# Kernel tuning notes

Measured on AMD Instinct MI355X. Metric: run time of the kernel, lower is better.

## Reference

```python
import jax, jax.numpy as jnp
import numpy as np

B = 8192
I = 1024
H = 1024


def setup_inputs() -> dict:
    key = jax.random.key(0)
    ks = jax.random.split(key, 7)
    s_in = 1.0 / np.sqrt(I)
    s_h = 1.0 / np.sqrt(H)
    return {
        "x_current": jax.random.normal(ks[0], (B, I), dtype=jnp.float32),
        "c_previous": jax.random.normal(ks[1], (B, H), dtype=jnp.float32),
        "h_previous": jax.random.normal(ks[2], (B, H), dtype=jnp.float32),
        # stacked gate weights, order (i, f, o, g); equivalent to 8 small nn.Linear
        "Wx": jax.random.normal(ks[3], (4 * H, I), dtype=jnp.float32) * s_in,
        "bx": jax.random.normal(ks[4], (4 * H,), dtype=jnp.float32) * s_in,
        "Wh": jax.random.normal(ks[5], (4 * H, H), dtype=jnp.float32) * s_h,
        "bh": jax.random.normal(ks[6], (4 * H,), dtype=jnp.float32) * s_h,
    }


def reference(x_current, c_previous, h_previous, Wx, bx, Wh, bh):
    # two fused GEMMs covering all 8 original linears: [B, 4H]
    gates = (jnp.einsum("bi,gi->bg", x_current, Wx) + bx
             + jnp.einsum("bh,gh->bg", h_previous, Wh) + bh)
    i_g, f_g, o_g, g_g = jnp.split(gates, 4, axis=-1)
    input_gate = jax.nn.sigmoid(i_g)
    forget_gate = jax.nn.sigmoid(f_g)
    output_gate = jax.nn.sigmoid(o_g)
    g_current = jnp.tanh(g_g)
    c_current = forget_gate * c_previous + input_gate * g_current
    h_current = output_gate * jnp.tanh(c_current)
    return (c_current, h_current)
```

## Files before the change

### kernel.cpp

```cpp
#include <hip/hip_runtime.h>
#include <hip/hip_bf16.h>

#define Bsz 8192
#define Isz 1024
#define Hsz 1024
#define Ksz 2048
#define Nsz 4096

#define BM 256
#define BN 256
#define BK 64
#define NT (Ksz / BK)

typedef __attribute__((ext_vector_type(8))) short bf16x8;
typedef __attribute__((ext_vector_type(4))) float f32x4;
typedef __attribute__((ext_vector_type(8))) unsigned short ushort8;

__device__ __forceinline__ void async_copy16(const void* g, void* l) {
  __builtin_amdgcn_global_load_lds(
      (const __attribute__((address_space(1))) void*)g,
      (__attribute__((address_space(3))) void*)l, 16, 0, 0);
}

__device__ __forceinline__ float sigmoid_f(float x) {
  return 1.0f / (1.0f + __expf(-x));
}
__device__ __forceinline__ float tanh_f(float x) {
  x = fminf(15.0f, fmaxf(-15.0f, x));
  const float e = __expf(-2.0f * x);
  return (1.0f - e) / (1.0f + e);
}

__device__ __forceinline__ unsigned short bfc(float f) {
  return __builtin_bit_cast(unsigned short, __float2bfloat16(f));
}
__device__ __forceinline__ ushort8 cvt8v(float4 v0, float4 v1) {
  ushort8 o;
  o[0] = bfc(v0.x); o[1] = bfc(v0.y); o[2] = bfc(v0.z); o[3] = bfc(v0.w);
  o[4] = bfc(v1.x); o[5] = bfc(v1.y); o[6] = bfc(v1.z); o[7] = bfc(v1.w);
  return o;
}

__global__ __launch_bounds__(256) void prep_kernel(
    const float* __restrict__ x, const float* __restrict__ h,
    const float* __restrict__ Wx, const float* __restrict__ Wh,
    const float* __restrict__ bx, const float* __restrict__ bh,
    __hip_bfloat16* __restrict__ Abf, __hip_bfloat16* __restrict__ Wbf,
    float* __restrict__ bsum) {
  const int idx = blockIdx.x * 256 + threadIdx.x;
  const int ATH = (Bsz * Ksz) / 8;
  if (idx < ATH) {
    const int b = idx >> 8;
    const int k = (idx & 255) << 3;
    const float* src = (k < Isz) ? (x + (size_t)b * Isz + k)
                                 : (h + (size_t)b * Hsz + (k - Isz));
    const float4 v0 = ((const float4*)src)[0];
    const float4 v1 = ((const float4*)src)[1];
    *(ushort8*)(Abf + (size_t)b * Ksz + k) = cvt8v(v0, v1);
  } else {
    const int t2 = idx - ATH;
    const int r = t2 >> 8;
    const int k = (t2 & 255) << 3;
    const int hh = r >> 2, g = r & 3;
    const float* src = (k < Isz) ? (Wx + (size_t)(g * Hsz + hh) * Isz + k)
                                 : (Wh + (size_t)(g * Hsz + hh) * Hsz + (k - Isz));
    const float4 v0 = ((const float4*)src)[0];
    const float4 v1 = ((const float4*)src)[1];
    *(ushort8*)(Wbf + (size_t)r * Ksz + k) = cvt8v(v0, v1);
  }
  if (idx < Nsz) {
    const int hh = idx >> 2, g = idx & 3;
    bsum[idx] = bx[g * Hsz + hh] + bh[g * Hsz + hh];
  }
}

__global__ __launch_bounds__(512, 2) void lstm_gemm_kernel(
    const __hip_bfloat16* __restrict__ A,
    const __hip_bfloat16* __restrict__ W,
    const float* __restrict__ bsum,
    const float* __restrict__ c_prev,
    float* __restrict__ c_out,
    float* __restrict__ h_out) {
  __shared__ ulong2 smem_raw[8192];
  __hip_bfloat16* const As = (__hip_bfloat16*)smem_raw;
  __hip_bfloat16* const Bs = As + 2 * BM * BK;
  char* const smemc = (char*)smem_raw;

  const int tid = threadIdx.x;
  const int lane = tid & 63;
  const int wave = tid >> 6;
  const int wm = wave >> 2;
  const int wn = wave & 3;

  const int orig = blockIdx.x;
  const int swz = (orig & 7) * 64 + (orig >> 3);
  const int bx = swz & 31;
  const int by = swz >> 5;
  const int row0 = bx * BM;
  const int col0 = by * BN;

  const __hip_bfloat16* const Ag = A + (size_t)row0 * Ksz;
  const __hip_bfloat16* const Wg = W + (size_t)col0 * Ksz;

  const int sr = tid >> 3;
  const int so = ((tid & 7) ^ (sr & 7)) << 3;

  auto stage = [&](const __hip_bfloat16* gsrc ,
                   char* lhalf ) {
#pragma unroll
    for (int p = 0; p < 2; ++p)
      async_copy16(gsrc + (size_t)(sr + p * 64) * Ksz,
                   lhalf + (tid + p * 512) * 16);
  };

  const int q = lane >> 4;
  const int cl = lane & 15;
  const int phi = cl & 7;
  const int swz0 = ((0 + q) ^ phi) << 3;
  const int swz1 = ((4 + q) ^ phi) << 3;
  const int aoff0 = (wm * 128 + cl) * BK + swz0;
  const int aoff1 = (wm * 128 + cl) * BK + swz1;
  const int boff0 = (wn * 64 + cl) * BK + swz0;
  const int boff1 = (wn * 64 + cl) * BK + swz1;

  stage(Ag + so, smemc);
  stage(Ag + (size_t)128 * Ksz + so, smemc + 16384);
  stage(Wg + so, smemc + 65536);
  stage(Wg + (size_t)128 * Ksz + so, smemc + 65536 + 16384);
  __builtin_amdgcn_sched_barrier(0);
  stage(Wg + BK + so, smemc + 65536 + 32768);
  stage(Wg + BK + (size_t)128 * Ksz + so, smemc + 65536 + 32768 + 16384);
  asm volatile("s_waitcnt vmcnt(4)" ::: "memory");
  __builtin_amdgcn_sched_barrier(0);
  __builtin_amdgcn_s_barrier();
  asm volatile("" ::: "memory");
  __builtin_amdgcn_sched_barrier(0);

  f32x4 acc[8][4] = {};

  for (int t = 0; t < NT; ++t) {
    const __hip_bfloat16* const Asb = As + (t & 1) * (BM * BK);
    const __hip_bfloat16* const Bsb = Bs + (t & 1) * (BM * BK);
    char* const nA = smemc + (((t + 1) & 1) * 32768);
    char* const nB = smemc + 65536 + ((t & 1) * 32768);
    const int kA = (t + 1) * BK;
    const int kB = (t + 2) * BK;
    const bool doA = (t + 1) < NT;
    const bool doB = (t + 2) < NT;

    bf16x8 bfr[4][2];

#pragma unroll
    for (int ph = 0; ph < 4; ++ph) {
      const int m0 = 2 * ph;
      bf16x8 a00 = *(const bf16x8*)(Asb + aoff0 + m0 * (16 * BK));
      bf16x8 a01 = *(const bf16x8*)(Asb + aoff1 + m0 * (16 * BK));
      bf16x8 a10 = *(const bf16x8*)(Asb + aoff0 + (m0 + 1) * (16 * BK));
      bf16x8 a11 = *(const bf16x8*)(Asb + aoff1 + (m0 + 1) * (16 * BK));
      if (ph == 0) {
#pragma unroll
        for (int n = 0; n < 4; ++n) {
          bfr[n][0] = *(const bf16x8*)(Bsb + boff0 + n * (16 * BK));
          bfr[n][1] = *(const bf16x8*)(Bsb + boff1 + n * (16 * BK));
        }
      }
      if (ph == 0 && doA) stage(Ag + kA + so, nA);
      if (ph == 1 && doA) stage(Ag + kA + (size_t)128 * Ksz + so, nA + 16384);
      if (ph == 2 && doB) stage(Wg + kB + so, nB);
      if (ph == 3 && doB) stage(Wg + kB + (size_t)128 * Ksz + so, nB + 16384);

      __builtin_amdgcn_sched_barrier(0);
      __builtin_amdgcn_s_barrier();
      asm volatile("" ::: "memory");
      __builtin_amdgcn_sched_barrier(0);

      __builtin_amdgcn_s_setprio(1);
#pragma unroll
      for (int n = 0; n < 4; ++n) {
        acc[m0][n]     = __builtin_amdgcn_mfma_f32_16x16x32_bf16(a00, bfr[n][0], acc[m0][n], 0, 0, 0);
        acc[m0][n]     = __builtin_amdgcn_mfma_f32_16x16x32_bf16(a01, bfr[n][1], acc[m0][n], 0, 0, 0);
        acc[m0 + 1][n] = __builtin_amdgcn_mfma_f32_16x16x32_bf16(a10, bfr[n][0], acc[m0 + 1][n], 0, 0, 0);
        acc[m0 + 1][n] = __builtin_amdgcn_mfma_f32_16x16x32_bf16(a11, bfr[n][1], acc[m0 + 1][n], 0, 0, 0);
      }
      __builtin_amdgcn_s_setprio(0);
      __builtin_amdgcn_sched_barrier(0);
      if (ph == 3) {
        if (t < NT - 2) {
          asm volatile("s_waitcnt vmcnt(4)" ::: "memory");
        } else if (t == NT - 2) {
          asm volatile("s_waitcnt vmcnt(0)" ::: "memory");
        }
      }
      __builtin_amdgcn_s_barrier();
      asm volatile("" ::: "memory");
      __builtin_amdgcn_sched_barrier(0);
    }
  }

  __syncthreads();
  float* const E = (float*)smem_raw + wave * (16 * 68);

  float bj[4];
#pragma unroll
  for (int n = 0; n < 4; ++n)
    bj[n] = bsum[col0 + wn * 64 + n * 16 + cl];

  const int hw = (col0 >> 2) + wn * 16;
  const int r16 = lane >> 2;
  const int tt = lane & 3;

#pragma unroll
  for (int i = 0; i < 8; ++i) {
#pragma unroll
    for (int n = 0; n < 4; ++n)
#pragma unroll
      for (int r = 0; r < 4; ++r)
        E[(q * 4 + r) * 68 + n * 16 + cl] = acc[i][n][r] + bj[n];
    __builtin_amdgcn_wave_barrier();
    const float* Er = E + r16 * 68 + tt * 16;
    const float4 f0 = ((const float4*)Er)[0];
    const float4 f1 = ((const float4*)Er)[1];
    const float4 f2 = ((const float4*)Er)[2];
    const float4 f3 = ((const float4*)Er)[3];

    const int row = row0 + wm * 128 + i * 16 + r16;
    const size_t off = (size_t)row * Hsz + hw + tt * 4;
    const float4 cp4 = *(const float4*)(c_prev + off);
    float4 c4, h4;
    {
      const float cn = sigmoid_f(f0.y) * cp4.x + sigmoid_f(f0.x) * tanh_f(f0.w);
      c4.x = cn; h4.x = sigmoid_f(f0.z) * tanh_f(cn);
    }
    {
      const float cn = sigmoid_f(f1.y) * cp4.y + sigmoid_f(f1.x) * tanh_f(f1.w);
      c4.y = cn; h4.y = sigmoid_f(f1.z) * tanh_f(cn);
    }
    {
      const float cn = sigmoid_f(f2.y) * cp4.z + sigmoid_f(f2.x) * tanh_f(f2.w);
      c4.z = cn; h4.z = sigmoid_f(f2.z) * tanh_f(cn);
    }
    {
      const float cn = sigmoid_f(f3.y) * cp4.w + sigmoid_f(f3.x) * tanh_f(f3.w);
      c4.w = cn; h4.w = sigmoid_f(f3.z) * tanh_f(cn);
    }
    *(float4*)(c_out + off) = c4;
    *(float4*)(h_out + off) = h4;
    __builtin_amdgcn_wave_barrier();
  }
}

extern "C" void kernel_launch(void* const* d_in, const int* in_sizes, int n_in,
                              void* d_out, int out_size, void* d_ws,
                              size_t ws_size, hipStream_t stream) {
  (void)in_sizes; (void)n_in; (void)out_size; (void)ws_size;
  const float* x  = (const float*)d_in[0];
  const float* cp = (const float*)d_in[1];
  const float* hp = (const float*)d_in[2];
  const float* Wx = (const float*)d_in[3];
  const float* bx = (const float*)d_in[4];
  const float* Wh = (const float*)d_in[5];
  const float* bh = (const float*)d_in[6];

  __hip_bfloat16* Abf = (__hip_bfloat16*)d_ws;
  __hip_bfloat16* Wbf = Abf + (size_t)Bsz * Ksz;
  float* bsum = (float*)(Wbf + (size_t)Nsz * Ksz);

  float* c_out = (float*)d_out;
  float* h_out = c_out + (size_t)Bsz * Hsz;

  const int total_threads = (Bsz * Ksz) / 8 + (Nsz * Ksz) / 8;
  prep_kernel<<<total_threads / 256, 256, 0, stream>>>(x, hp, Wx, Wh, bx, bh,
                                                       Abf, Wbf, bsum);
  dim3 grid(Bsz / BM * (Nsz / BN));
  lstm_gemm_kernel<<<grid, 512, 0, stream>>>(Abf, Wbf, bsum, cp, c_out, h_out);
}
```

Before: 310.3 us.

## Software-pipeline A fragment loads and cut GEMM barriers per K tile

The GEMM main loop is restructured so each K tile issues two workgroup barriers instead of eight. A fragments are double-buffered in registers (even and odd sets), so the LDS reads for the next MFMA cluster are issued before the current cluster runs. Async global-to-LDS staging is spread across the clusters, with one mid-tile barrier guarding reuse of the B buffer. Separately, sigmoid and tanh in the epilogue use the hardware reciprocal instead of a full divide, trading a little accuracy for fewer instructions.

```diff
diff --git a/kernel.cpp b/kernel.cpp
--- a/kernel.cpp
+++ b/kernel.cpp
@@ -22,13 +22,16 @@
       (__attribute__((address_space(3))) void*)l, 16, 0, 0);
 }
 
+__device__ __forceinline__ float fast_rcp(float x) {
+  return __builtin_amdgcn_rcpf(x);
+}
 __device__ __forceinline__ float sigmoid_f(float x) {
-  return 1.0f / (1.0f + __expf(-x));
+  return fast_rcp(1.0f + __expf(-x));
 }
 __device__ __forceinline__ float tanh_f(float x) {
   x = fminf(15.0f, fmaxf(-15.0f, x));
   const float e = __expf(-2.0f * x);
-  return (1.0f - e) / (1.0f + e);
+  return (1.0f - e) * fast_rcp(1.0f + e);
 }
 
 __device__ __forceinline__ unsigned short bfc(float f) {
@@ -105,8 +108,7 @@
   const int sr = tid >> 3;
   const int so = ((tid & 7) ^ (sr & 7)) << 3;
 
-  auto stage = [&](const __hip_bfloat16* gsrc ,
-                   char* lhalf ) {
+  auto stage = [&](const __hip_bfloat16* gsrc, char* lhalf) {
 #pragma unroll
     for (int p = 0; p < 2; ++p)
       async_copy16(gsrc + (size_t)(sr + p * 64) * Ksz,
@@ -130,13 +132,33 @@
   __builtin_amdgcn_sched_barrier(0);
   stage(Wg + BK + so, smemc + 65536 + 32768);
   stage(Wg + BK + (size_t)128 * Ksz + so, smemc + 65536 + 32768 + 16384);
+  __builtin_amdgcn_sched_barrier(0);
   asm volatile("s_waitcnt vmcnt(4)" ::: "memory");
+  __builtin_amdgcn_s_barrier();
   __builtin_amdgcn_sched_barrier(0);
-  __builtin_amdgcn_s_barrier();
-  asm volatile("" ::: "memory");
-  __builtin_amdgcn_sched_barrier(0);
 
   f32x4 acc[8][4] = {};
+
+#define LDA(dst, m)                                                        \
+  dst[0][0] = *(const bf16x8*)(Asb + aoff0 + (m) * (16 * BK));             \
+  dst[0][1] = *(const bf16x8*)(Asb + aoff1 + (m) * (16 * BK));             \
+  dst[1][0] = *(const bf16x8*)(Asb + aoff0 + ((m) + 1) * (16 * BK));       \
+  dst[1][1] = *(const bf16x8*)(Asb + aoff1 + ((m) + 1) * (16 * BK));
+
+#define CLUSTER(mi, p)                                                     \
+  __builtin_amdgcn_s_setprio(1);                                           \
+  _Pragma("unroll")                                                        \
+  for (int n = 0; n < 4; ++n) {                                            \
+    acc[mi][n] = __builtin_amdgcn_mfma_f32_16x16x32_bf16(                  \
+        p[0][0], b0[n][0], acc[mi][n], 0, 0, 0);                           \
+    acc[mi][n] = __builtin_amdgcn_mfma_f32_16x16x32_bf16(                  \
+        p[0][1], b0[n][1], acc[mi][n], 0, 0, 0);                           \
+    acc[(mi) + 1][n] = __builtin_amdgcn_mfma_f32_16x16x32_bf16(            \
+        p[1][0], b0[n][0], acc[(mi) + 1][n], 0, 0, 0);                     \
+    acc[(mi) + 1][n] = __builtin_amdgcn_mfma_f32_16x16x32_bf16(            \
+        p[1][1], b0[n][1], acc[(mi) + 1][n], 0, 0, 0);                     \
+  }                                                                        \
+  __builtin_amdgcn_s_setprio(0);
 
   for (int t = 0; t < NT; ++t) {
     const __hip_bfloat16* const Asb = As + (t & 1) * (BM * BK);
@@ -148,54 +170,48 @@
     const bool doA = (t + 1) < NT;
     const bool doB = (t + 2) < NT;
 
-    bf16x8 bfr[4][2];
-
-#pragma unroll
-    for (int ph = 0; ph < 4; ++ph) {
-      const int m0 = 2 * ph;
-      bf16x8 a00 = *(const bf16x8*)(Asb + aoff0 + m0 * (16 * BK));
-      bf16x8 a01 = *(const bf16x8*)(Asb + aoff1 + m0 * (16 * BK));
-      bf16x8 a10 = *(const bf16x8*)(Asb + aoff0 + (m0 + 1) * (16 * BK));
-      bf16x8 a11 = *(const bf16x8*)(Asb + aoff1 + (m0 + 1) * (16 * BK));
-      if (ph == 0) {
-#pragma unroll
-        for (int n = 0; n < 4; ++n) {
-          bfr[n][0] = *(const bf16x8*)(Bsb + boff0 + n * (16 * BK));
-          bfr[n][1] = *(const bf16x8*)(Bsb + boff1 + n * (16 * BK));
-        }
-      }
-      if (ph == 0 && doA) stage(Ag + kA + so, nA);
-      if (ph == 1 && doA) stage(Ag + kA + (size_t)128 * Ksz + so, nA + 16384);
-      if (ph == 2 && doB) stage(Wg + kB + so, nB);
-      if (ph == 3 && doB) stage(Wg + kB + (size_t)128 * Ksz + so, nB + 16384);
-
-      __builtin_amdgcn_sched_barrier(0);
-      __builtin_amdgcn_s_barrier();
-      asm volatile("" ::: "memory");
-      __builtin_amdgcn_sched_barrier(0);
-
-      __builtin_amdgcn_s_setprio(1);
-#pragma unroll
-      for (int n = 0; n < 4; ++n) {
-        acc[m0][n]     = __builtin_amdgcn_mfma_f32_16x16x32_bf16(a00, bfr[n][0], acc[m0][n], 0, 0, 0);
-        acc[m0][n]     = __builtin_amdgcn_mfma_f32_16x16x32_bf16(a01, bfr[n][1], acc[m0][n], 0, 0, 0);
-        acc[m0 + 1][n] = __builtin_amdgcn_mfma_f32_16x16x32_bf16(a10, bfr[n][0], acc[m0 + 1][n], 0, 0, 0);
-        acc[m0 + 1][n] = __builtin_amdgcn_mfma_f32_16x16x32_bf16(a11, bfr[n][1], acc[m0 + 1][n], 0, 0, 0);
-      }
-      __builtin_amdgcn_s_setprio(0);
-      __builtin_amdgcn_sched_barrier(0);
-      if (ph == 3) {
-        if (t < NT - 2) {
-          asm volatile("s_waitcnt vmcnt(4)" ::: "memory");
-        } else if (t == NT - 2) {
-          asm volatile("s_waitcnt vmcnt(0)" ::: "memory");
-        }
-      }
-      __builtin_amdgcn_s_barrier();
-      asm volatile("" ::: "memory");
-      __builtin_amdgcn_sched_barrier(0);
-    }
-  }
+    bf16x8 b0[4][2];
+    bf16x8 aE[2][2], aO[2][2];
+
+#pragma unroll
+    for (int n = 0; n < 4; ++n) {
+      b0[n][0] = *(const bf16x8*)(Bsb + boff0 + n * (16 * BK));
+      b0[n][1] = *(const bf16x8*)(Bsb + boff1 + n * (16 * BK));
+    }
+    LDA(aE, 0)
+
+    LDA(aO, 2)
+    if (doA) stage(Ag + kA + so, nA);
+    __builtin_amdgcn_sched_barrier(0);
+    CLUSTER(0, aE)
+
+    LDA(aE, 4)
+    if (doA) stage(Ag + kA + (size_t)128 * Ksz + so, nA + 16384);
+    __builtin_amdgcn_sched_barrier(0);
+    CLUSTER(2, aO)
+
+    __builtin_amdgcn_s_barrier();
+    __builtin_amdgcn_sched_barrier(0);
+
+    LDA(aO, 6)
+    if (doB) stage(Wg + kB + so, nB);
+    __builtin_amdgcn_sched_barrier(0);
+    CLUSTER(4, aE)
+
+    if (doB) stage(Wg + kB + (size_t)128 * Ksz + so, nB + 16384);
+    __builtin_amdgcn_sched_barrier(0);
+    CLUSTER(6, aO)
+
+    if (t < NT - 2) {
+      asm volatile("s_waitcnt vmcnt(4)" ::: "memory");
+    } else if (t == NT - 2) {
+      asm volatile("s_waitcnt vmcnt(0)" ::: "memory");
+    }
+    __builtin_amdgcn_s_barrier();
+    __builtin_amdgcn_sched_barrier(0);
+  }
+#undef LDA
+#undef CLUSTER
 
   __syncthreads();
   float* const E = (float*)smem_raw + wave * (16 * 68);
```

New measurement: 294.5 us. 5.1% less time.
